# Kernel tuning notes

Measured on AMD Instinct MI355X. Metric: run time of the kernel, lower is better.

## Reference

```python
import jax, jax.numpy as jnp
import numpy as np

N_NODES = 50000
N_EDGES = 800000
C_IN = 128
HEADS = 4
C_HEAD = 32  # c_out // heads = 128 // 4
NEG_SLOPE = 0.2


def setup_inputs() -> dict:
    key = jax.random.key(0)
    k_x, k_e, k_w, k_as, k_ad, k_b = jax.random.split(key, 6)
    x = jax.random.normal(k_x, (N_NODES, C_IN), dtype=jnp.float32)
    edge_index = jax.random.randint(k_e, (2, N_EDGES), 0, N_NODES, dtype=jnp.int64)
    # xavier_uniform_ with gain=1.414 on lin.weight [H*C, C_IN] -> same bound for W [C_IN, H*C]
    bound = 1.414 * np.sqrt(6.0 / (C_IN + HEADS * C_HEAD))
    W = jax.random.uniform(k_w, (C_IN, HEADS * C_HEAD), minval=-bound, maxval=bound, dtype=jnp.float32)
    # glorot init for attention vectors (PyG default)
    ab = np.sqrt(6.0 / (1 + HEADS * C_HEAD))
    att_src = jax.random.uniform(k_as, (HEADS, C_HEAD), minval=-ab, maxval=ab, dtype=jnp.float32)
    att_dst = jax.random.uniform(k_ad, (HEADS, C_HEAD), minval=-ab, maxval=ab, dtype=jnp.float32)
    bias = jnp.zeros((HEADS * C_HEAD,), dtype=jnp.float32)
    return {"x": x, "edge_index": edge_index, "W": W,
            "att_src": att_src, "att_dst": att_dst, "bias": bias}


def reference(x, edge_index, W, att_src, att_dst, bias):
    N = x.shape[0]
    H, C = att_src.shape
    # Linear projection, per-head split: [N, H, C]
    xl = (x @ W).reshape(N, H, C)
    a_src = jnp.einsum('nhc,hc->nh', xl, att_src)  # [N, H]
    a_dst = jnp.einsum('nhc,hc->nh', xl, att_dst)  # [N, H]

    src, dst = edge_index[0], edge_index[1]
    loop = jnp.arange(N, dtype=edge_index.dtype)
    # GATConv(add_self_loops=True): remove existing self loops, then add one per node.
    src_f = jnp.concatenate([src, loop])  # [E+N]
    dst_f = jnp.concatenate([dst, loop])
    drop = jnp.concatenate([src == dst, jnp.zeros((N,), dtype=bool)])

    e = jax.nn.leaky_relu(a_src[src_f] + a_dst[dst_f], NEG_SLOPE)  # [E+N, H]
    e = jnp.where(drop[:, None], -jnp.inf, e)

    # segment softmax over edges sharing a destination (every node has a self loop -> max is finite)
    m = jax.ops.segment_max(e, dst_f, num_segments=N)          # [N, H]
    ex = jnp.exp(e - m[dst_f])                                  # [E+N, H]
    denom = jax.ops.segment_sum(ex, dst_f, num_segments=N)     # [N, H]
    alpha = ex / denom[dst_f]                                   # [E+N, H]

    msg = xl[src_f] * alpha[:, :, None]                         # [E+N, H, C]
    out = jax.ops.segment_sum(msg, dst_f, num_segments=N)      # [N, H, C]
    out = out.reshape(N, H * C) + bias
    return out / jnp.sqrt(jnp.asarray(H, dtype=out.dtype))
```

## Files before the change

kernel.cpp:

```cpp
#include <hip/hip_runtime.h>
#include <math.h>

#define CDIM 128
#define HEADS 4
#define NEG 0.2f

typedef __attribute__((ext_vector_type(8))) short bf16x8;
typedef __attribute__((ext_vector_type(8))) unsigned short u16x8;
typedef __attribute__((ext_vector_type(4))) float f32x4;

static __device__ __forceinline__ unsigned short f2bf(float f) {
    unsigned u = __float_as_uint(f);
    u += 0x7FFFu + ((u >> 16) & 1u);
    return (unsigned short)(u >> 16);
}
static __device__ __forceinline__ float bf2f(unsigned short s) {
    return __uint_as_float((unsigned)s << 16);
}

#define LDS_STRIDE 136

__global__ __launch_bounds__(256) void gemm_mfma_kernel(const float* __restrict__ x,
                                                        const float* __restrict__ W,
                                                        const float* __restrict__ att_src,
                                                        const float* __restrict__ att_dst,
                                                        unsigned short* __restrict__ xlh,
                                                        float* __restrict__ a_src,
                                                        float* __restrict__ a_dst, int N) {
    __shared__ unsigned short As[64 * LDS_STRIDE];
    __shared__ unsigned short Bs[128 * LDS_STRIDE];
    const int tid = threadIdx.x;
    const int row0 = blockIdx.x * 64;

#pragma unroll
    for (int i = 0; i < 8; ++i) {
        int f = tid + i * 256;
        int r = f >> 5, k4 = f & 31;
        float4 v = make_float4(0.f, 0.f, 0.f, 0.f);
        int gr = row0 + r;
        if (gr < N) v = *(const float4*)(x + (size_t)gr * CDIM + k4 * 4);
        ushort4 h;
        h.x = f2bf(v.x); h.y = f2bf(v.y); h.z = f2bf(v.z); h.w = f2bf(v.w);
        *(ushort4*)(&As[r * LDS_STRIDE + k4 * 4]) = h;
    }
#pragma unroll
    for (int i = 0; i < 16; ++i) {
        int f = tid + i * 256;
        int k = f >> 5, c4 = (f & 31) * 4;
        float4 v = *(const float4*)(W + (size_t)k * CDIM + c4);
        Bs[(c4 + 0) * LDS_STRIDE + k] = f2bf(v.x);
        Bs[(c4 + 1) * LDS_STRIDE + k] = f2bf(v.y);
        Bs[(c4 + 2) * LDS_STRIDE + k] = f2bf(v.z);
        Bs[(c4 + 3) * LDS_STRIDE + k] = f2bf(v.w);
    }
    __syncthreads();

    const int wave = tid >> 6;
    const int lane = tid & 63;
    const int m    = lane & 15;
    const int quad = lane >> 4;
    const int wrow = wave * 16;

    bf16x8 a[4];
#pragma unroll
    for (int ks = 0; ks < 4; ++ks)
        a[ks] = *(const bf16x8*)(&As[(wrow + m) * LDS_STRIDE + ks * 32 + quad * 8]);

    f32x4 acc[8];
#pragma unroll
    for (int t = 0; t < 8; ++t) {
        f32x4 c = {0.f, 0.f, 0.f, 0.f};
#pragma unroll
        for (int ks = 0; ks < 4; ++ks) {
            bf16x8 b = *(const bf16x8*)(&Bs[(t * 16 + m) * LDS_STRIDE + ks * 32 + quad * 8]);
            c = __builtin_amdgcn_mfma_f32_16x16x32_bf16(a[ks], b, c, 0, 0, 0);
        }
        acc[t] = c;
    }

#pragma unroll
    for (int t = 0; t < 8; ++t) {
#pragma unroll
        for (int reg = 0; reg < 4; ++reg) {
            int row = row0 + wrow + quad * 4 + reg;
            if (row < N) xlh[(size_t)row * CDIM + t * 16 + m] = f2bf(acc[t][reg]);
        }
    }

    float ps[4][4], pd[4][4];
#pragma unroll
    for (int h = 0; h < 4; ++h)
#pragma unroll
        for (int reg = 0; reg < 4; ++reg) { ps[h][reg] = 0.f; pd[h][reg] = 0.f; }
#pragma unroll
    for (int t = 0; t < 8; ++t) {
        int h = t >> 1;
        float vs = att_src[t * 16 + m];
        float vd = att_dst[t * 16 + m];
#pragma unroll
        for (int reg = 0; reg < 4; ++reg) {
            ps[h][reg] += acc[t][reg] * vs;
            pd[h][reg] += acc[t][reg] * vd;
        }
    }
#pragma unroll
    for (int off = 8; off > 0; off >>= 1) {
#pragma unroll
        for (int h = 0; h < 4; ++h)
#pragma unroll
            for (int reg = 0; reg < 4; ++reg) {
                ps[h][reg] += __shfl_down(ps[h][reg], off, 16);
                pd[h][reg] += __shfl_down(pd[h][reg], off, 16);
            }
    }
    if (m == 0) {
#pragma unroll
        for (int reg = 0; reg < 4; ++reg) {
            int row = row0 + wrow + quad * 4 + reg;
            if (row < N) {
#pragma unroll
                for (int h = 0; h < 4; ++h) {
                    a_src[row * 4 + h] = ps[h][reg];
                    a_dst[row * 4 + h] = pd[h][reg];
                }
            }
        }
    }
}

__global__ __launch_bounds__(256) void hist_kernel(const int* __restrict__ src,
                                                   const int* __restrict__ dst,
                                                   int* __restrict__ counts,
                                                   int* __restrict__ rank, int E) {
    int e = blockIdx.x * 256 + threadIdx.x;
    if (e >= E) return;
    int s = src[e], d = dst[e];
    if (s != d) rank[e] = atomicAdd(&counts[d], 1);
}

__global__ __launch_bounds__(256) void reduce_kernel(const int* __restrict__ counts,
                                                     int* __restrict__ blockSums, int N) {
    __shared__ int sh[256];
    int idx = blockIdx.x * 256 + threadIdx.x;
    sh[threadIdx.x] = (idx < N) ? counts[idx] : 0;
    __syncthreads();
    for (int off = 128; off > 0; off >>= 1) {
        if (threadIdx.x < off) sh[threadIdx.x] += sh[threadIdx.x + off];
        __syncthreads();
    }
    if (threadIdx.x == 0) blockSums[blockIdx.x] = sh[0];
}

__global__ __launch_bounds__(256) void scan_top_kernel(int* __restrict__ blockSums,
                                                       int* __restrict__ blockPrefix, int nb) {
    __shared__ int sh[256];
    int t = threadIdx.x;
    sh[t] = (t < nb) ? blockSums[t] : 0;
    __syncthreads();
    for (int off = 1; off < 256; off <<= 1) {
        int v = (t >= off) ? sh[t - off] : 0;
        __syncthreads();
        sh[t] += v;
        __syncthreads();
    }
    if (t < nb) blockPrefix[t] = (t == 0) ? 0 : sh[t - 1];
}

__global__ __launch_bounds__(256) void apply_kernel(const int* __restrict__ counts,
                                                    const int* __restrict__ blockPrefix,
                                                    int* __restrict__ offsets, int N) {
    __shared__ int sh[256];
    int idx = blockIdx.x * 256 + threadIdx.x;
    int t = threadIdx.x;
    int c = (idx < N) ? counts[idx] : 0;
    sh[t] = c;
    __syncthreads();
    for (int off = 1; off < 256; off <<= 1) {
        int v = (t >= off) ? sh[t - off] : 0;
        __syncthreads();
        sh[t] += v;
        __syncthreads();
    }
    if (idx < N) offsets[idx] = sh[t] - c + blockPrefix[blockIdx.x];
}

__global__ __launch_bounds__(256) void scatter_kernel(const int* __restrict__ src,
                                                      const int* __restrict__ dst,
                                                      const int* __restrict__ offsets,
                                                      const int* __restrict__ rank,
                                                      int* __restrict__ bucket, int E) {
    int e = blockIdx.x * 256 + threadIdx.x;
    if (e >= E) return;
    int s = src[e], d = dst[e];
    if (s == d) return;
    bucket[offsets[d] + rank[e]] = s;
}

__global__ __launch_bounds__(256) void gather_kernel(const int* __restrict__ offsets,
                                                     const int* __restrict__ counts,
                                                     const int* __restrict__ bucket,
                                                     const unsigned short* __restrict__ xlh,
                                                     const float* __restrict__ a_src,
                                                     const float* __restrict__ a_dst,
                                                     const float* __restrict__ bias,
                                                     float* __restrict__ out, int N) {
    const int node = blockIdx.x * 16 + (threadIdx.x >> 4);
    const int lane16 = threadIdx.x & 15;
    if (node >= N) return;
    const int c8 = lane16 * 8;
    const int h = lane16 >> 2;

    const float ad = a_dst[node * 4 + h];
    const int beg = offsets[node];
    const int cnt = counts[node];

    float acc[8];
#pragma unroll
    for (int i = 0; i < 8; ++i) acc[i] = 0.f;
    float den = 0.f;

    int j = 0;
    for (; j + 4 <= cnt; j += 4) {
        int s0 = bucket[beg + j + 0];
        int s1 = bucket[beg + j + 1];
        int s2 = bucket[beg + j + 2];
        int s3 = bucket[beg + j + 3];
        float e0 = a_src[s0 * 4 + h] + ad;
        float e1 = a_src[s1 * 4 + h] + ad;
        float e2 = a_src[s2 * 4 + h] + ad;
        float e3 = a_src[s3 * 4 + h] + ad;
        u16x8 u0 = *(const u16x8*)(xlh + (size_t)s0 * CDIM + c8);
        u16x8 u1 = *(const u16x8*)(xlh + (size_t)s1 * CDIM + c8);
        u16x8 u2 = *(const u16x8*)(xlh + (size_t)s2 * CDIM + c8);
        u16x8 u3 = *(const u16x8*)(xlh + (size_t)s3 * CDIM + c8);
        e0 = e0 > 0.f ? e0 : NEG * e0;
        e1 = e1 > 0.f ? e1 : NEG * e1;
        e2 = e2 > 0.f ? e2 : NEG * e2;
        e3 = e3 > 0.f ? e3 : NEG * e3;
        float w0 = __expf(e0), w1 = __expf(e1), w2 = __expf(e2), w3 = __expf(e3);
#pragma unroll
        for (int i = 0; i < 8; ++i) {
            acc[i] += w0 * bf2f(u0[i]) + w1 * bf2f(u1[i])
                    + w2 * bf2f(u2[i]) + w3 * bf2f(u3[i]);
        }
        den += w0 + w1 + w2 + w3;
    }
    for (; j < cnt; ++j) {
        int s = bucket[beg + j];
        float e = a_src[s * 4 + h] + ad;
        u16x8 u = *(const u16x8*)(xlh + (size_t)s * CDIM + c8);
        e = e > 0.f ? e : NEG * e;
        float w = __expf(e);
#pragma unroll
        for (int i = 0; i < 8; ++i) acc[i] += w * bf2f(u[i]);
        den += w;
    }
    float es = a_src[node * 4 + h] + ad;
    es = es > 0.f ? es : NEG * es;
    float ws = __expf(es);
    u16x8 u = *(const u16x8*)(xlh + (size_t)node * CDIM + c8);
#pragma unroll
    for (int i = 0; i < 8; ++i) acc[i] += ws * bf2f(u[i]);
    den += ws;

    float inv = 1.0f / den;
    float4 b0 = *(const float4*)(bias + c8);
    float4 b1 = *(const float4*)(bias + c8 + 4);
    float4 o0, o1;
    o0.x = (acc[0] * inv + b0.x) * 0.5f;
    o0.y = (acc[1] * inv + b0.y) * 0.5f;
    o0.z = (acc[2] * inv + b0.z) * 0.5f;
    o0.w = (acc[3] * inv + b0.w) * 0.5f;
    o1.x = (acc[4] * inv + b1.x) * 0.5f;
    o1.y = (acc[5] * inv + b1.y) * 0.5f;
    o1.z = (acc[6] * inv + b1.z) * 0.5f;
    o1.w = (acc[7] * inv + b1.w) * 0.5f;
    *(float4*)(out + (size_t)node * CDIM + c8) = o0;
    *(float4*)(out + (size_t)node * CDIM + c8 + 4) = o1;
}

extern "C" void kernel_launch(void* const* d_in, const int* in_sizes, int n_in,
                              void* d_out, int out_size, void* d_ws, size_t ws_size,
                              hipStream_t stream) {
    const float* x       = (const float*)d_in[0];
    const int*   ei      = (const int*)d_in[1];
    const float* W       = (const float*)d_in[2];
    const float* att_src = (const float*)d_in[3];
    const float* att_dst = (const float*)d_in[4];
    const float* bias    = (const float*)d_in[5];
    float* out = (float*)d_out;

    const int N = in_sizes[0] / CDIM;
    const int E = in_sizes[1] / 2;
    const int nb = (N + 255) / 256;

    char* wsb = (char*)d_ws;
    unsigned short* xlh = (unsigned short*)wsb;         wsb += (size_t)N * CDIM * sizeof(unsigned short);
    float* a_src = (float*)wsb;                         wsb += (size_t)N * HEADS * sizeof(float);
    float* a_dst = (float*)wsb;                         wsb += (size_t)N * HEADS * sizeof(float);
    int* counts  = (int*)wsb;                           wsb += (size_t)N * sizeof(int);
    int* offsets = (int*)wsb;                           wsb += (size_t)N * sizeof(int);
    int* blockSums   = (int*)wsb;                       wsb += (size_t)nb * sizeof(int);
    int* blockPrefix = (int*)wsb;                       wsb += (size_t)nb * sizeof(int);
    int* rank    = (int*)wsb;                           wsb += (size_t)E * sizeof(int);
    int* bucket  = (int*)wsb;                           wsb += (size_t)E * sizeof(int);

    hipMemsetAsync(counts, 0, (size_t)N * sizeof(int), stream);

    gemm_mfma_kernel<<<(N + 63) / 64, 256, 0, stream>>>(x, W, att_src, att_dst, xlh, a_src, a_dst, N);
    hist_kernel<<<(E + 255) / 256, 256, 0, stream>>>(ei, ei + E, counts, rank, E);
    reduce_kernel<<<nb, 256, 0, stream>>>(counts, blockSums, N);
    scan_top_kernel<<<1, 256, 0, stream>>>(blockSums, blockPrefix, nb);
    apply_kernel<<<nb, 256, 0, stream>>>(counts, blockPrefix, offsets, N);
    scatter_kernel<<<(E + 255) / 256, 256, 0, stream>>>(ei, ei + E, offsets, rank, bucket, E);
    gather_kernel<<<(N + 15) / 16, 256, 0, stream>>>(offsets, counts, bucket, xlh, a_src, a_dst, bias, out, N);
}
```

Baseline: 201.7 us.

## Fuse histogram into GEMM launch, collapse scan to one kernel, unroll gather by 8

Histogram blocks are appended to the GEMM grid so edge counting overlaps the projection in a single launch. The three-kernel prefix scan is replaced by one kernel where each block claims its base with an atomic cursor; segments stay disjoint but are no longer in node order. The gather loop processes eight neighbours per iteration to raise memory-level parallelism. The cost is that histogram blocks carry the GEMM's large LDS allocation, which may limit their occupancy, and the wider unroll raises register pressure.

```diff
diff --git a/kernel.cpp b/kernel.cpp
--- a/kernel.cpp
+++ b/kernel.cpp
@@ -20,15 +20,30 @@
 
 #define LDS_STRIDE 136
 
-__global__ __launch_bounds__(256) void gemm_mfma_kernel(const float* __restrict__ x,
+__global__ __launch_bounds__(256) void gemm_hist_kernel(const float* __restrict__ x,
                                                         const float* __restrict__ W,
                                                         const float* __restrict__ att_src,
                                                         const float* __restrict__ att_dst,
                                                         unsigned short* __restrict__ xlh,
                                                         float* __restrict__ a_src,
-                                                        float* __restrict__ a_dst, int N) {
+                                                        float* __restrict__ a_dst, int N,
+                                                        const int* __restrict__ esrc,
+                                                        const int* __restrict__ edst,
+                                                        int* __restrict__ counts,
+                                                        int* __restrict__ rank, int E,
+                                                        int gemmBlocks) {
     __shared__ unsigned short As[64 * LDS_STRIDE];
     __shared__ unsigned short Bs[128 * LDS_STRIDE];
+
+    if (blockIdx.x >= gemmBlocks) {
+        int e = (blockIdx.x - gemmBlocks) * 256 + threadIdx.x;
+        if (e < E) {
+            int s = esrc[e], d = edst[e];
+            if (s != d) rank[e] = atomicAdd(&counts[d], 1);
+        }
+        return;
+    }
+
     const int tid = threadIdx.x;
     const int row0 = blockIdx.x * 64;
 
@@ -128,48 +143,11 @@
     }
 }
 
-__global__ __launch_bounds__(256) void hist_kernel(const int* __restrict__ src,
-                                                   const int* __restrict__ dst,
-                                                   int* __restrict__ counts,
-                                                   int* __restrict__ rank, int E) {
-    int e = blockIdx.x * 256 + threadIdx.x;
-    if (e >= E) return;
-    int s = src[e], d = dst[e];
-    if (s != d) rank[e] = atomicAdd(&counts[d], 1);
-}
-
-__global__ __launch_bounds__(256) void reduce_kernel(const int* __restrict__ counts,
-                                                     int* __restrict__ blockSums, int N) {
+__global__ __launch_bounds__(256) void scan_fused_kernel(const int* __restrict__ counts,
+                                                         int* __restrict__ offsets,
+                                                         int* __restrict__ cursor, int N) {
     __shared__ int sh[256];
-    int idx = blockIdx.x * 256 + threadIdx.x;
-    sh[threadIdx.x] = (idx < N) ? counts[idx] : 0;
-    __syncthreads();
-    for (int off = 128; off > 0; off >>= 1) {
-        if (threadIdx.x < off) sh[threadIdx.x] += sh[threadIdx.x + off];
-        __syncthreads();
-    }
-    if (threadIdx.x == 0) blockSums[blockIdx.x] = sh[0];
-}
-
-__global__ __launch_bounds__(256) void scan_top_kernel(int* __restrict__ blockSums,
-                                                       int* __restrict__ blockPrefix, int nb) {
-    __shared__ int sh[256];
-    int t = threadIdx.x;
-    sh[t] = (t < nb) ? blockSums[t] : 0;
-    __syncthreads();
-    for (int off = 1; off < 256; off <<= 1) {
-        int v = (t >= off) ? sh[t - off] : 0;
-        __syncthreads();
-        sh[t] += v;
-        __syncthreads();
-    }
-    if (t < nb) blockPrefix[t] = (t == 0) ? 0 : sh[t - 1];
-}
-
-__global__ __launch_bounds__(256) void apply_kernel(const int* __restrict__ counts,
-                                                    const int* __restrict__ blockPrefix,
-                                                    int* __restrict__ offsets, int N) {
-    __shared__ int sh[256];
+    __shared__ int baseSh;
     int idx = blockIdx.x * 256 + threadIdx.x;
     int t = threadIdx.x;
     int c = (idx < N) ? counts[idx] : 0;
@@ -181,7 +159,9 @@
         sh[t] += v;
         __syncthreads();
     }
-    if (idx < N) offsets[idx] = sh[t] - c + blockPrefix[blockIdx.x];
+    if (t == 255) baseSh = atomicAdd(cursor, sh[255]);
+    __syncthreads();
+    if (idx < N) offsets[idx] = baseSh + sh[t] - c;
 }
 
 __global__ __launch_bounds__(256) void scatter_kernel(const int* __restrict__ src,
@@ -220,30 +200,28 @@
     float den = 0.f;
 
     int j = 0;
-    for (; j + 4 <= cnt; j += 4) {
-        int s0 = bucket[beg + j + 0];
-        int s1 = bucket[beg + j + 1];
-        int s2 = bucket[beg + j + 2];
-        int s3 = bucket[beg + j + 3];
-        float e0 = a_src[s0 * 4 + h] + ad;
-        float e1 = a_src[s1 * 4 + h] + ad;
-        float e2 = a_src[s2 * 4 + h] + ad;
-        float e3 = a_src[s3 * 4 + h] + ad;
-        u16x8 u0 = *(const u16x8*)(xlh + (size_t)s0 * CDIM + c8);
-        u16x8 u1 = *(const u16x8*)(xlh + (size_t)s1 * CDIM + c8);
-        u16x8 u2 = *(const u16x8*)(xlh + (size_t)s2 * CDIM + c8);
-        u16x8 u3 = *(const u16x8*)(xlh + (size_t)s3 * CDIM + c8);
-        e0 = e0 > 0.f ? e0 : NEG * e0;
-        e1 = e1 > 0.f ? e1 : NEG * e1;
-        e2 = e2 > 0.f ? e2 : NEG * e2;
-        e3 = e3 > 0.f ? e3 : NEG * e3;
-        float w0 = __expf(e0), w1 = __expf(e1), w2 = __expf(e2), w3 = __expf(e3);
-#pragma unroll
-        for (int i = 0; i < 8; ++i) {
-            acc[i] += w0 * bf2f(u0[i]) + w1 * bf2f(u1[i])
-                    + w2 * bf2f(u2[i]) + w3 * bf2f(u3[i]);
-        }
-        den += w0 + w1 + w2 + w3;
+    for (; j + 8 <= cnt; j += 8) {
+        int s[8];
+#pragma unroll
+        for (int q = 0; q < 8; ++q) s[q] = bucket[beg + j + q];
+        float e[8];
+#pragma unroll
+        for (int q = 0; q < 8; ++q) e[q] = a_src[s[q] * 4 + h] + ad;
+        u16x8 u[8];
+#pragma unroll
+        for (int q = 0; q < 8; ++q) u[q] = *(const u16x8*)(xlh + (size_t)s[q] * CDIM + c8);
+        float w[8];
+#pragma unroll
+        for (int q = 0; q < 8; ++q) {
+            float eq = e[q] > 0.f ? e[q] : NEG * e[q];
+            w[q] = __expf(eq);
+        }
+#pragma unroll
+        for (int q = 0; q < 8; ++q) {
+#pragma unroll
+            for (int i = 0; i < 8; ++i) acc[i] += w[q] * bf2f(u[q][i]);
+            den += w[q];
+        }
     }
     for (; j < cnt; ++j) {
         int s = bucket[beg + j];
@@ -299,19 +277,18 @@
     float* a_src = (float*)wsb;                         wsb += (size_t)N * HEADS * sizeof(float);
     float* a_dst = (float*)wsb;                         wsb += (size_t)N * HEADS * sizeof(float);
     int* counts  = (int*)wsb;                           wsb += (size_t)N * sizeof(int);
+    int* cursor  = (int*)wsb;                           wsb += sizeof(int);
     int* offsets = (int*)wsb;                           wsb += (size_t)N * sizeof(int);
-    int* blockSums   = (int*)wsb;                       wsb += (size_t)nb * sizeof(int);
-    int* blockPrefix = (int*)wsb;                       wsb += (size_t)nb * sizeof(int);
     int* rank    = (int*)wsb;                           wsb += (size_t)E * sizeof(int);
     int* bucket  = (int*)wsb;                           wsb += (size_t)E * sizeof(int);
 
-    hipMemsetAsync(counts, 0, (size_t)N * sizeof(int), stream);
-
-    gemm_mfma_kernel<<<(N + 63) / 64, 256, 0, stream>>>(x, W, att_src, att_dst, xlh, a_src, a_dst, N);
-    hist_kernel<<<(E + 255) / 256, 256, 0, stream>>>(ei, ei + E, counts, rank, E);
-    reduce_kernel<<<nb, 256, 0, stream>>>(counts, blockSums, N);
-    scan_top_kernel<<<1, 256, 0, stream>>>(blockSums, blockPrefix, nb);
-    apply_kernel<<<nb, 256, 0, stream>>>(counts, blockPrefix, offsets, N);
+    hipMemsetAsync(counts, 0, ((size_t)N + 1) * sizeof(int), stream);
+
+    const int gemmBlocks = (N + 63) / 64;
+    const int histBlocks = (E + 255) / 256;
+    gemm_hist_kernel<<<gemmBlocks + histBlocks, 256, 0, stream>>>(
+        x, W, att_src, att_dst, xlh, a_src, a_dst, N, ei, ei + E, counts, rank, E, gemmBlocks);
+    scan_fused_kernel<<<nb, 256, 0, stream>>>(counts, offsets, cursor, N);
     scatter_kernel<<<(E + 255) / 256, 256, 0, stream>>>(ei, ei + E, offsets, rank, bucket, E);
     gather_kernel<<<(N + 15) / 16, 256, 0, stream>>>(offsets, counts, bucket, xlh, a_src, a_dst, bias, out, N);
 }
```

Result: faster. 194.1 us (-3.8%).
